# Kernel optimization log

Hardware: AMD Instinct MI355X
Metric: run time of the kernel (lower is better)

The kernel has to match this reference:

```python
import jax, jax.numpy as jnp
import numpy as np

A_ANCHORS = 102400
BATCH = 16
N_ANN = 32
OMEGA = 3.0
EPSILON = 2.0
WING_C = OMEGA - OMEGA * float(np.log(1.0 + OMEGA / EPSILON))


def _calc_iou(a, b):
    # a: [A,4] anchors, b: [N,4] gt boxes -> [A,N]
    area = (b[:, 2] - b[:, 0]) * (b[:, 3] - b[:, 1])
    iw = jnp.minimum(a[:, 2][:, None], b[None, :, 2]) - jnp.maximum(a[:, 0][:, None], b[None, :, 0])
    ih = jnp.minimum(a[:, 3][:, None], b[None, :, 3]) - jnp.maximum(a[:, 1][:, None], b[None, :, 1])
    iw = jnp.clip(iw, 0.0)
    ih = jnp.clip(ih, 0.0)
    ua = ((a[:, 2] - a[:, 0]) * (a[:, 3] - a[:, 1]))[:, None] + area[None, :] - iw * ih
    ua = jnp.clip(ua, 1e-8)
    return iw * ih / ua


def setup_inputs() -> dict:
    rng = np.random.default_rng(0)
    B, N, A = BATCH, N_ANN, A_ANCHORS
    x1 = rng.uniform(1.0, 500.0, (B, N)).astype(np.float32)
    y1 = rng.uniform(1.0, 500.0, (B, N)).astype(np.float32)
    w = rng.uniform(16.0, 100.0, (B, N)).astype(np.float32)
    h = rng.uniform(16.0, 100.0, (B, N)).astype(np.float32)
    boxes = np.stack([x1, y1, x1 + w, y1 + h], axis=-1)
    # last 12 annotations per image are padding (first coord <= 0)
    boxes[:, 20:, 0] -= 600.0
    boxes[:, 20:, 2] -= 600.0
    ldm = rng.uniform(0.0, 640.0, (B, N, 196)).astype(np.float32)
    ldm[:, ::5, :] = 0.0  # some faces have no landmark annotation
    annotations = np.concatenate([boxes, ldm], axis=-1)
    ax1 = rng.uniform(0.0, 560.0, (A,)).astype(np.float32)
    ay1 = rng.uniform(0.0, 560.0, (A,)).astype(np.float32)
    aw = rng.uniform(16.0, 80.0, (A,)).astype(np.float32)
    ah = rng.uniform(16.0, 80.0, (A,)).astype(np.float32)
    anchor = np.stack([ax1, ay1, ax1 + aw, ay1 + ah], axis=-1)
    # plant jittered copies of valid GT boxes so IoU>=0.7 positives exist
    slot = 0
    for j in range(B):
        for k in range(20):
            for _ in range(4):
                anchor[slot] = boxes[j, k] + rng.uniform(-1.5, 1.5, (4,)).astype(np.float32)
                slot += 1
    anchors = anchor[None, :, :]
    k1, k2, k3 = jax.random.split(jax.random.key(0), 3)
    return {
        "classifications": jax.random.normal(k1, (B, A, 2), jnp.float32),
        "bbox_regressions": jax.random.normal(k2, (B, A, 4), jnp.float32),
        "ldm_regressions": jax.random.normal(k3, (B, A, 196), jnp.float32),
        "anchors": jnp.asarray(anchors),
        "annotations": jnp.asarray(annotations),
    }


def reference(classifications, bbox_regressions, ldm_regressions, anchors, annotations):
    anchor = anchors[0]
    A = anchor.shape[0]
    aw = anchor[:, 2] - anchor[:, 0]
    ah = anchor[:, 3] - anchor[:, 1]
    acx = anchor[:, 0] + 0.5 * aw
    acy = anchor[:, 1] + 0.5 * ah
    bbox_scale = jnp.array([0.1, 0.1, 0.2, 0.2], jnp.float32)
    even = (jnp.arange(196) % 2) == 0
    ctr = jnp.where(even, acx[:, None], acy[:, None])         # [A,196]
    den = jnp.where(even, aw[:, None], ah[:, None]) + 1e-14   # [A,196]
    s = jnp.concatenate([jnp.ones(68, jnp.float32), 3.0 * jnp.ones(128, jnp.float32)])
    arange_A = jnp.arange(A)

    def per_sample(cls, breg, lreg, ann):
        valid = ann[:, 0] > 0
        boxes = ann[:, :4]
        ldm_ann = ann[:, 4:]
        has_gt = jnp.any(valid)
        iou = _calc_iou(anchor, boxes)
        iou = jnp.where(valid[None, :], iou, -1.0)  # mask invalid GT
        iou_max = iou.max(axis=1)
        iou_arg = iou.argmax(axis=1)
        neg = iou_max < 0.4
        pos = iou_max >= 0.7
        npos = pos.sum()
        nneg = neg.sum()
        # hard-negative mining: keep top-(3*npos) negative scores
        keep = jnp.minimum(nneg, 3 * npos)
        neg_losses = jnp.where(neg, -cls[:, 1], -jnp.inf)
        sorted_neg = jnp.sort(neg_losses)[::-1]
        neg_mean = jnp.where(arange_A < keep, sorted_neg, 0.0).sum() / jnp.maximum(keep, 1)
        pos_mean = jnp.where(pos, -cls[:, 0], 0.0).sum() / jnp.maximum(npos, 1)
        cls_loss = jnp.where(has_gt & (npos > 0), pos_mean + neg_mean, 0.0)
        gb = boxes[iou_arg]
        gw = gb[:, 2] - gb[:, 0]
        gh = gb[:, 3] - gb[:, 1]
        gcx = gb[:, 0] + 0.5 * gw
        gcy = gb[:, 1] + 0.5 * gh
        tdx = (gcx - acx) / (aw + 1e-14)
        tdy = (gcy - acy) / (ah + 1e-14)
        tdw = jnp.log(gw / aw)
        tdh = jnp.log(gh / ah)
        btgt = jnp.stack([tdx, tdy, tdw, tdh], axis=1) / bbox_scale
        d = jnp.abs(btgt - breg)
        sl1 = jnp.where(d < 1.0, 0.5 * d * d, d - 0.5)
        bbox_loss = jnp.where(
            has_gt & (npos > 0),
            jnp.where(pos[:, None], sl1, 0.0).sum() / (jnp.maximum(npos, 1) * 4),
            0.0,
        )
        # landmark wing loss over positive anchors whose GT has landmarks
        gl = ldm_ann[iou_arg]  # [A,196]
        lpos = pos & (gl.sum(axis=1) > 0)
        nl = lpos.sum()
        ltgt = (gl - ctr) / den / 0.1
        dd = jnp.abs(ltgt * s - lreg * s)
        wing = jnp.where(dd < OMEGA, OMEGA * jnp.log1p(dd / EPSILON), dd - WING_C)
        ldm_loss = jnp.where(
            has_gt & (nl > 0),
            jnp.where(lpos[:, None], wing, 0.0).sum() / (jnp.maximum(nl, 1) * 196),
            0.0,
        )
        return cls_loss, bbox_loss, ldm_loss

    return jax.vmap(per_sample)(classifications, bbox_regressions, ldm_regressions, annotations)
```

## Files before the change

kernel.cpp:

```cpp
#include <hip/hip_runtime.h>

#define A_ANCH 102400
#define BATCH  16
#define N_ANN  32
#define NLDM   196
#define ANNW   200
#define BLOCKS_PER 400
#define NSLOT  32
#define SEL_T  1024
#define CAP    14336

#define OFF_PCNT   (16u << 10)
#define OFF_PSUM   (131072u)
#define OFF_HSLOT  (294912u)
#define OFF_KEYS   (1u << 20)
#define OFF_SPILL  (8u << 20)

__device__ __forceinline__ float key_to_val(unsigned kk) {
    unsigned vb = (kk & 0x80000000u) ? (kk ^ 0x80000000u) : ~kk;
    return __uint_as_float(vb);
}

__global__ __launch_bounds__(256) void k_main(
    const float* __restrict__ cls,
    const float* __restrict__ breg,
    const float* __restrict__ lreg,
    const float* __restrict__ anchors,
    const float* __restrict__ ann,
    int4* __restrict__ pcnt,
    double* __restrict__ psum,
    unsigned* __restrict__ keys,
    unsigned* __restrict__ histS)
{
    const int tid = threadIdx.x;
    const int b = blockIdx.x / BLOCKS_PER;
    const int blk = blockIdx.x % BLOCKS_PER;
    const int a = blk * 256 + tid;

    __shared__ int    bh[256];
    __shared__ int    s_cnt[4][3];
    __shared__ double s_sum[4][3];
    bh[tid] = 0;
    __syncthreads();

    float4 av = *reinterpret_cast<const float4*>(anchors + (size_t)a * 4);
    const float aw = av.z - av.x, ah = av.w - av.y;
    const float areaA = aw * ah;

    const float* __restrict__ annb = ann + (size_t)b * N_ANN * ANNW;
    float bnum = -1e30f, bden = 1.0f; int arg = 0;
    #pragma unroll 8
    for (int j = 0; j < N_ANN; ++j) {
        float4 bx = *reinterpret_cast<const float4*>(annb + (size_t)j * ANNW);
        float areaB = (bx.z - bx.x) * (bx.w - bx.y);
        float iw = fminf(av.z, bx.z) - fmaxf(av.x, bx.x);
        float ih = fminf(av.w, bx.w) - fmaxf(av.y, bx.y);
        iw = fmaxf(iw, 0.0f); ih = fmaxf(ih, 0.0f);
        float inter = iw * ih;
        float ua = fmaxf(areaA + areaB - inter, 1e-8f);
        bool upd = inter * bden > bnum * ua;
        bnum = upd ? inter : bnum;
        bden = upd ? ua : bden;
        arg  = upd ? j : arg;
    }
    const bool pos = bnum >= 0.7f * bden;
    const bool neg = bnum <  0.4f * bden;

    float2 c = *reinterpret_cast<const float2*>(cls + ((size_t)b * A_ANCH + a) * 2);

    float nv = -c.y;
    unsigned bits = __float_as_uint(nv);
    unsigned key = (bits & 0x80000000u) ? ~bits : (bits ^ 0x80000000u);
    keys[(size_t)b * A_ANCH + a] = neg ? key : 0u;
    if (neg) atomicAdd(&bh[key >> 24], 1);

    double v_pos = 0.0, v_bb = 0.0, v_ldm = 0.0;
    float glsum = 0.0f;
    const float acx = av.x + 0.5f * aw, acy = av.y + 0.5f * ah;

    if (pos) {
        v_pos = (double)(-c.x);

        float4 gb = *reinterpret_cast<const float4*>(annb + (size_t)arg * ANNW);
        float gw = gb.z - gb.x, gh = gb.w - gb.y;
        float gcx = gb.x + 0.5f * gw, gcy = gb.y + 0.5f * gh;
        float t0 = ((gcx - acx) / (aw + 1e-14f)) / 0.1f;
        float t1 = ((gcy - acy) / (ah + 1e-14f)) / 0.1f;
        float t2 = logf(gw / aw) / 0.2f;
        float t3 = logf(gh / ah) / 0.2f;

        float4 rv = *reinterpret_cast<const float4*>(breg + ((size_t)b * A_ANCH + a) * 4);
        float bsum = 0.0f, d;
        d = fabsf(t0 - rv.x); bsum += (d < 1.0f) ? 0.5f * d * d : d - 0.5f;
        d = fabsf(t1 - rv.y); bsum += (d < 1.0f) ? 0.5f * d * d : d - 0.5f;
        d = fabsf(t2 - rv.z); bsum += (d < 1.0f) ? 0.5f * d * d : d - 0.5f;
        d = fabsf(t3 - rv.w); bsum += (d < 1.0f) ? 0.5f * d * d : d - 0.5f;
        v_bb = (double)bsum;

        const float* gl = annb + (size_t)arg * ANNW + 4;
        for (int i = 0; i < NLDM; i += 4) {
            float4 g4 = *reinterpret_cast<const float4*>(gl + i);
            glsum += g4.x + g4.y + g4.z + g4.w;
        }
    }
    const bool lpos = pos && (glsum > 0.0f);
    if (lpos) {
        const float* gl = annb + (size_t)arg * ANNW + 4;
        const float* lr = lreg + ((size_t)b * A_ANCH + a) * NLDM;
        const float inv_aw = 1.0f / ((aw + 1e-14f) * 0.1f);
        const float inv_ah = 1.0f / ((ah + 1e-14f) * 0.1f);
        double wsum = 0.0;
        for (int i = 0; i < NLDM; i += 4) {
            float4 l4 = *reinterpret_cast<const float4*>(lr + i);
            float4 g4 = *reinterpret_cast<const float4*>(gl + i);
            float s = (i < 68) ? 1.0f : 3.0f;
            float lt0 = (g4.x - acx) * inv_aw;
            float lt1 = (g4.y - acy) * inv_ah;
            float lt2 = (g4.z - acx) * inv_aw;
            float lt3 = (g4.w - acy) * inv_ah;
            float d0 = fabsf(lt0 * s - l4.x * s);
            float d1 = fabsf(lt1 * s - l4.y * s);
            float d2 = fabsf(lt2 * s - l4.z * s);
            float d3 = fabsf(lt3 * s - l4.w * s);
            float w0 = (d0 < 3.0f) ? 3.0f * log1pf(d0 * 0.5f) : d0 - 0.25112780437753474f;
            float w1 = (d1 < 3.0f) ? 3.0f * log1pf(d1 * 0.5f) : d1 - 0.25112780437753474f;
            float w2 = (d2 < 3.0f) ? 3.0f * log1pf(d2 * 0.5f) : d2 - 0.25112780437753474f;
            float w3 = (d3 < 3.0f) ? 3.0f * log1pf(d3 * 0.5f) : d3 - 0.25112780437753474f;
            wsum += (double)w0 + (double)w1 + (double)w2 + (double)w3;
        }
        v_ldm = wsum;
    }

    unsigned long long bp = __ballot(pos);
    unsigned long long bn = __ballot(neg);
    unsigned long long bl = __ballot(lpos);
    const int wave = tid >> 6, lane = tid & 63;
    if (lane == 0) {
        s_cnt[wave][0] = (int)__popcll(bp);
        s_cnt[wave][1] = (int)__popcll(bn);
        s_cnt[wave][2] = (int)__popcll(bl);
    }
    if (bp) {
        #pragma unroll
        for (int off = 32; off > 0; off >>= 1) {
            v_pos += __shfl_down(v_pos, off);
            v_bb  += __shfl_down(v_bb, off);
            v_ldm += __shfl_down(v_ldm, off);
        }
    }
    if (lane == 0) {
        s_sum[wave][0] = v_pos;
        s_sum[wave][1] = v_bb;
        s_sum[wave][2] = v_ldm;
    }
    __syncthreads();
    if (tid == 0) {
        int np = s_cnt[0][0] + s_cnt[1][0] + s_cnt[2][0] + s_cnt[3][0];
        int nn = s_cnt[0][1] + s_cnt[1][1] + s_cnt[2][1] + s_cnt[3][1];
        int nl = s_cnt[0][2] + s_cnt[1][2] + s_cnt[2][2] + s_cnt[3][2];
        pcnt[b * BLOCKS_PER + blk] = make_int4(np, nn, nl, 0);
        size_t pbase = (size_t)(b * BLOCKS_PER + blk) * 3;
        psum[pbase + 0] = s_sum[0][0] + s_sum[1][0] + s_sum[2][0] + s_sum[3][0];
        psum[pbase + 1] = s_sum[0][1] + s_sum[1][1] + s_sum[2][1] + s_sum[3][1];
        psum[pbase + 2] = s_sum[0][2] + s_sum[1][2] + s_sum[2][2] + s_sum[3][2];
    }
    if (bh[tid]) {
        unsigned slot = (unsigned)(blockIdx.x & (NSLOT - 1));
        atomicAdd(&histS[((unsigned)b * NSLOT + slot) * 256u + (unsigned)tid],
                  (unsigned)bh[tid]);
    }
}

__global__ __launch_bounds__(SEL_T) void k_sel(
    const float* __restrict__ ann,
    const int4* __restrict__ pcnt,
    const double* __restrict__ psum,
    const unsigned* __restrict__ histS,
    const unsigned* __restrict__ keys,
    unsigned* __restrict__ spill,
    float* __restrict__ out)
{
    const int b = blockIdx.x;
    const int tid = threadIdx.x;
    const int wave = tid >> 6, lane = tid & 63;

    __shared__ unsigned shist[256];
    __shared__ unsigned s_cand[CAP];
    __shared__ int    sredi[16][3];
    __shared__ double sredd[16][3];
    __shared__ int    s_i[8];
    __shared__ double s_d[4];
    __shared__ unsigned s_prefix;
    __shared__ int s_r;
    __shared__ int s_cc;

    if (tid < 256) {
        unsigned h = 0;
        #pragma unroll
        for (int s = 0; s < NSLOT; ++s)
            h += histS[((unsigned)b * NSLOT + s) * 256u + (unsigned)tid];
        shist[tid] = h;
    }

    int np = 0, nn = 0, nl = 0;
    double a0 = 0.0, a1 = 0.0, a2 = 0.0;
    for (int i = tid; i < BLOCKS_PER; i += SEL_T) {
        int4 p = pcnt[b * BLOCKS_PER + i];
        np += p.x; nn += p.y; nl += p.z;
        size_t pbase = (size_t)(b * BLOCKS_PER + i) * 3;
        a0 += psum[pbase + 0]; a1 += psum[pbase + 1]; a2 += psum[pbase + 2];
    }
    #pragma unroll
    for (int off = 32; off > 0; off >>= 1) {
        np += __shfl_down(np, off); nn += __shfl_down(nn, off); nl += __shfl_down(nl, off);
        a0 += __shfl_down(a0, off); a1 += __shfl_down(a1, off); a2 += __shfl_down(a2, off);
    }
    if (lane == 0) {
        sredi[wave][0] = np; sredi[wave][1] = nn; sredi[wave][2] = nl;
        sredd[wave][0] = a0; sredd[wave][1] = a1; sredd[wave][2] = a2;
    }

    if (tid < 64) {
        bool v = (tid < N_ANN) && (ann[(size_t)(b * N_ANN + tid) * ANNW] > 0.0f);
        unsigned long long bm = __ballot(v);
        if (tid == 0) s_i[6] = (bm != 0ull) ? 1 : 0;
    }
    __syncthreads();

    if (tid == 0) {
        int tnp = 0, tnn = 0, tnl = 0; double t0 = 0, t1 = 0, t2 = 0;
        for (int w = 0; w < 16; ++w) {
            tnp += sredi[w][0]; tnn += sredi[w][1]; tnl += sredi[w][2];
            t0 += sredd[w][0]; t1 += sredd[w][1]; t2 += sredd[w][2];
        }
        int keep = min(tnn, 3 * tnp);
        int bin0 = -1, rem = 0;
        if (keep > 0) {
            unsigned cum = 0;
            for (int i = 255; i >= 0; --i) {
                unsigned cc = shist[i];
                if (cum + cc >= (unsigned)keep) { bin0 = i; rem = keep - (int)cum; break; }
                cum += cc;
            }
        }
        s_i[0] = tnp; s_i[1] = tnn; s_i[2] = tnl;
        s_i[3] = keep; s_i[4] = bin0; s_i[5] = rem;
        s_d[0] = t0; s_d[1] = t1; s_d[2] = t2;
        s_cc = 0;
    }
    __syncthreads();

    const int keep = s_i[3];
    const int bin0 = s_i[4];
    unsigned* sp = spill + (size_t)b * A_ANCH;

    double lneg = 0.0;
    if (keep > 0) {
        const uint4* k4 = reinterpret_cast<const uint4*>(keys + (size_t)b * A_ANCH);
        const unsigned long long lmask = (1ull << lane) - 1ull;
        for (int i = tid; i < A_ANCH / 4; i += SEL_T) {
            uint4 kv = k4[i];
            #pragma unroll
            for (int e = 0; e < 4; ++e) {
                unsigned kk = (e == 0) ? kv.x : (e == 1) ? kv.y : (e == 2) ? kv.z : kv.w;
                int top = (int)(kk >> 24);
                if (top > bin0) lneg += (double)key_to_val(kk);
                bool m = (top == bin0);
                unsigned long long bm = __ballot(m);
                if (bm) {
                    int ldr = __ffsll((long long)bm) - 1;
                    int base = 0;
                    if (lane == ldr) base = atomicAdd(&s_cc, (int)__popcll(bm));
                    base = __shfl(base, ldr);
                    if (m) {
                        int idx = base + (int)__popcll(bm & lmask);
                        if (idx < CAP) s_cand[idx] = kk;
                        else sp[idx - CAP] = kk;
                    }
                }
            }
        }
    }
    #pragma unroll
    for (int off = 32; off > 0; off >>= 1) lneg += __shfl_down(lneg, off);
    __syncthreads();
    if (lane == 0) sredd[wave][0] = lneg;
    __syncthreads();
    if (tid == 0) {
        double t = 0.0;
        for (int w = 0; w < 16; ++w) t += sredd[w][0];
        s_d[3] = t;
        s_i[7] = s_cc;
    }
    __syncthreads();
    const int cnt = s_i[7];

    unsigned prefix = ((unsigned)bin0) << 24;
    for (int pass = 1; pass < 4; ++pass) {
        const int shift = 24 - 8 * pass;
        const unsigned maskAbove = 0xFFFFFFFFu << (shift + 8);
        if (tid < 256) shist[tid] = 0;
        __syncthreads();
        for (int i = tid; i < cnt; i += SEL_T) {
            unsigned kk = (i < CAP) ? s_cand[i] : sp[i - CAP];
            if ((kk & maskAbove) == prefix)
                atomicAdd(&shist[(kk >> shift) & 0xFFu], 1u);
        }
        __syncthreads();
        if (tid == 0) {
            int rem = (pass == 1) ? s_i[5] : s_r;
            unsigned cum = 0;
            unsigned npre = prefix;
            int nrem = rem;
            for (int bin = 255; bin >= 0; --bin) {
                unsigned cc = shist[bin];
                if (cum + cc >= (unsigned)rem) {
                    nrem = rem - (int)cum;
                    npre = prefix | ((unsigned)bin << shift);
                    break;
                }
                cum += cc;
            }
            s_r = nrem; s_prefix = npre;
        }
        __syncthreads();
        prefix = s_prefix;
    }
    const unsigned T = prefix;

    double ls = 0.0;
    for (int i = tid; i < cnt; i += SEL_T) {
        unsigned kk = (i < CAP) ? s_cand[i] : sp[i - CAP];
        if (kk > T) ls += (double)key_to_val(kk);
    }
    #pragma unroll
    for (int off = 32; off > 0; off >>= 1) ls += __shfl_down(ls, off);
    __syncthreads();
    if (lane == 0) sredd[wave][0] = ls;
    __syncthreads();

    if (tid == 0) {
        double cs = 0.0;
        for (int w = 0; w < 16; ++w) cs += sredd[w][0];
        double total = s_d[3] + cs + (double)s_r * (double)key_to_val(T);

        const int npos = s_i[0], nlc = s_i[2], hasgt = s_i[6];
        double cls_l = 0.0, bbox_l = 0.0, ldm_l = 0.0;
        if (hasgt && npos > 0) {
            double neg_mean = (keep > 0) ? total / (double)keep : 0.0;
            cls_l = s_d[0] / (double)npos + neg_mean;
            bbox_l = s_d[1] / ((double)npos * 4.0);
        }
        if (hasgt && nlc > 0) {
            ldm_l = s_d[2] / ((double)nlc * 196.0);
        }
        out[b]             = (float)cls_l;
        out[BATCH + b]     = (float)bbox_l;
        out[2 * BATCH + b] = (float)ldm_l;
    }
}

extern "C" void kernel_launch(void* const* d_in, const int* in_sizes, int n_in,
                              void* d_out, int out_size, void* d_ws, size_t ws_size,
                              hipStream_t stream) {
    const float* cls     = (const float*)d_in[0];
    const float* breg    = (const float*)d_in[1];
    const float* lreg    = (const float*)d_in[2];
    const float* anchors = (const float*)d_in[3];
    const float* ann     = (const float*)d_in[4];

    char* ws = (char*)d_ws;
    int4*     pcnt  = (int4*)(ws + OFF_PCNT);
    double*   psum  = (double*)(ws + OFF_PSUM);
    unsigned* histS = (unsigned*)(ws + OFF_HSLOT);
    unsigned* keys  = (unsigned*)(ws + OFF_KEYS);
    unsigned* spill = (unsigned*)(ws + OFF_SPILL);
    float*    out   = (float*)d_out;

    hipMemsetAsync(histS, 0, (size_t)BATCH * NSLOT * 256 * 4, stream);
    hipLaunchKernelGGL(k_main, dim3(BATCH * BLOCKS_PER), dim3(256), 0, stream,
                       cls, breg, lreg, anchors, ann, pcnt, psum, keys, histS);
    hipLaunchKernelGGL(k_sel, dim3(BATCH), dim3(SEL_T), 0, stream,
                       ann, pcnt, psum, histS, keys, spill, out);
}
```

Before: 157.6 us.

## Fuse anchor-matching and hard-negative selection into one kernel via last-block-done

Merges the per-anchor loss kernel and the per-image top-k selection kernel into a single launch. Each block now loops over 1600 anchors (64 blocks per image) and writes its own histogram slice instead of doing global atomics. The last block to finish an image, detected with an atomic counter, performs the radix selection. The selection now runs with 256 threads instead of 1024 and keeps candidates in global memory rather than shared memory, which may slow the serial tail. The grid is also much smaller (1024 blocks), which could reduce parallelism in the memory-bound main phase.

Measured after the change: 333.2 us. 2.11x slower.

```diff
diff --git a/kernel.cpp b/kernel.cpp
--- a/kernel.cpp
+++ b/kernel.cpp
@@ -5,260 +5,236 @@
 #define N_ANN  32
 #define NLDM   196
 #define ANNW   200
-#define BLOCKS_PER 400
-#define NSLOT  32
-#define SEL_T  1024
-#define CAP    14336
-
-#define OFF_PCNT   (16u << 10)
-#define OFF_PSUM   (131072u)
-#define OFF_HSLOT  (294912u)
-#define OFF_KEYS   (1u << 20)
-#define OFF_SPILL  (8u << 20)
+#define NB     64
+#define APB    1600
+#define WING_CONST 0.25112780437753474f
+
+#define OFF_DONE   0u
+#define OFF_PCNT   4096u
+#define OFF_PSUM   (64u << 10)
+#define OFF_BHIST  (128u << 10)
+#define OFF_KEYS   (2u << 20)
+#define OFF_CAND   (16u << 20)
 
 __device__ __forceinline__ float key_to_val(unsigned kk) {
     unsigned vb = (kk & 0x80000000u) ? (kk ^ 0x80000000u) : ~kk;
     return __uint_as_float(vb);
 }
 
-__global__ __launch_bounds__(256) void k_main(
+__global__ __launch_bounds__(256, 4) void k_fused(
     const float* __restrict__ cls,
     const float* __restrict__ breg,
     const float* __restrict__ lreg,
     const float* __restrict__ anchors,
     const float* __restrict__ ann,
+    int* __restrict__ done,
     int4* __restrict__ pcnt,
     double* __restrict__ psum,
+    unsigned* __restrict__ bhist,
     unsigned* __restrict__ keys,
-    unsigned* __restrict__ histS)
+    unsigned* __restrict__ cand,
+    float* __restrict__ out)
 {
     const int tid = threadIdx.x;
-    const int b = blockIdx.x / BLOCKS_PER;
-    const int blk = blockIdx.x % BLOCKS_PER;
-    const int a = blk * 256 + tid;
+    const int b   = blockIdx.x / NB;
+    const int blk = blockIdx.x % NB;
+    const int base = blk * APB;
+    const int wave = tid >> 6, lane = tid & 63;
 
     __shared__ int    bh[256];
-    __shared__ int    s_cnt[4][3];
-    __shared__ double s_sum[4][3];
+    __shared__ int    sci[4][3];
+    __shared__ double scd[4][3];
+    __shared__ int    s_flag;
     bh[tid] = 0;
     __syncthreads();
 
-    float4 av = *reinterpret_cast<const float4*>(anchors + (size_t)a * 4);
-    const float aw = av.z - av.x, ah = av.w - av.y;
-    const float areaA = aw * ah;
-
     const float* __restrict__ annb = ann + (size_t)b * N_ANN * ANNW;
-    float bnum = -1e30f, bden = 1.0f; int arg = 0;
-    #pragma unroll 8
-    for (int j = 0; j < N_ANN; ++j) {
-        float4 bx = *reinterpret_cast<const float4*>(annb + (size_t)j * ANNW);
-        float areaB = (bx.z - bx.x) * (bx.w - bx.y);
-        float iw = fminf(av.z, bx.z) - fmaxf(av.x, bx.x);
-        float ih = fminf(av.w, bx.w) - fmaxf(av.y, bx.y);
-        iw = fmaxf(iw, 0.0f); ih = fmaxf(ih, 0.0f);
-        float inter = iw * ih;
-        float ua = fmaxf(areaA + areaB - inter, 1e-8f);
-        bool upd = inter * bden > bnum * ua;
-        bnum = upd ? inter : bnum;
-        bden = upd ? ua : bden;
-        arg  = upd ? j : arg;
-    }
-    const bool pos = bnum >= 0.7f * bden;
-    const bool neg = bnum <  0.4f * bden;
-
-    float2 c = *reinterpret_cast<const float2*>(cls + ((size_t)b * A_ANCH + a) * 2);
-
-    float nv = -c.y;
-    unsigned bits = __float_as_uint(nv);
-    unsigned key = (bits & 0x80000000u) ? ~bits : (bits ^ 0x80000000u);
-    keys[(size_t)b * A_ANCH + a] = neg ? key : 0u;
-    if (neg) atomicAdd(&bh[key >> 24], 1);
-
-    double v_pos = 0.0, v_bb = 0.0, v_ldm = 0.0;
-    float glsum = 0.0f;
-    const float acx = av.x + 0.5f * aw, acy = av.y + 0.5f * ah;
-
-    if (pos) {
-        v_pos = (double)(-c.x);
-
-        float4 gb = *reinterpret_cast<const float4*>(annb + (size_t)arg * ANNW);
-        float gw = gb.z - gb.x, gh = gb.w - gb.y;
-        float gcx = gb.x + 0.5f * gw, gcy = gb.y + 0.5f * gh;
-        float t0 = ((gcx - acx) / (aw + 1e-14f)) / 0.1f;
-        float t1 = ((gcy - acy) / (ah + 1e-14f)) / 0.1f;
-        float t2 = logf(gw / aw) / 0.2f;
-        float t3 = logf(gh / ah) / 0.2f;
-
-        float4 rv = *reinterpret_cast<const float4*>(breg + ((size_t)b * A_ANCH + a) * 4);
-        float bsum = 0.0f, d;
-        d = fabsf(t0 - rv.x); bsum += (d < 1.0f) ? 0.5f * d * d : d - 0.5f;
-        d = fabsf(t1 - rv.y); bsum += (d < 1.0f) ? 0.5f * d * d : d - 0.5f;
-        d = fabsf(t2 - rv.z); bsum += (d < 1.0f) ? 0.5f * d * d : d - 0.5f;
-        d = fabsf(t3 - rv.w); bsum += (d < 1.0f) ? 0.5f * d * d : d - 0.5f;
-        v_bb = (double)bsum;
-
-        const float* gl = annb + (size_t)arg * ANNW + 4;
-        for (int i = 0; i < NLDM; i += 4) {
-            float4 g4 = *reinterpret_cast<const float4*>(gl + i);
-            glsum += g4.x + g4.y + g4.z + g4.w;
-        }
-    }
-    const bool lpos = pos && (glsum > 0.0f);
-    if (lpos) {
-        const float* gl = annb + (size_t)arg * ANNW + 4;
-        const float* lr = lreg + ((size_t)b * A_ANCH + a) * NLDM;
-        const float inv_aw = 1.0f / ((aw + 1e-14f) * 0.1f);
-        const float inv_ah = 1.0f / ((ah + 1e-14f) * 0.1f);
-        double wsum = 0.0;
-        for (int i = 0; i < NLDM; i += 4) {
-            float4 l4 = *reinterpret_cast<const float4*>(lr + i);
-            float4 g4 = *reinterpret_cast<const float4*>(gl + i);
-            float s = (i < 68) ? 1.0f : 3.0f;
-            float lt0 = (g4.x - acx) * inv_aw;
-            float lt1 = (g4.y - acy) * inv_ah;
-            float lt2 = (g4.z - acx) * inv_aw;
-            float lt3 = (g4.w - acy) * inv_ah;
-            float d0 = fabsf(lt0 * s - l4.x * s);
-            float d1 = fabsf(lt1 * s - l4.y * s);
-            float d2 = fabsf(lt2 * s - l4.z * s);
-            float d3 = fabsf(lt3 * s - l4.w * s);
-            float w0 = (d0 < 3.0f) ? 3.0f * log1pf(d0 * 0.5f) : d0 - 0.25112780437753474f;
-            float w1 = (d1 < 3.0f) ? 3.0f * log1pf(d1 * 0.5f) : d1 - 0.25112780437753474f;
-            float w2 = (d2 < 3.0f) ? 3.0f * log1pf(d2 * 0.5f) : d2 - 0.25112780437753474f;
-            float w3 = (d3 < 3.0f) ? 3.0f * log1pf(d3 * 0.5f) : d3 - 0.25112780437753474f;
-            wsum += (double)w0 + (double)w1 + (double)w2 + (double)w3;
-        }
-        v_ldm = wsum;
-    }
-
-    unsigned long long bp = __ballot(pos);
-    unsigned long long bn = __ballot(neg);
-    unsigned long long bl = __ballot(lpos);
-    const int wave = tid >> 6, lane = tid & 63;
+
+    int np = 0, nn = 0, nl = 0;
+    double vp = 0.0, vb = 0.0, vl = 0.0;
+
+    #pragma unroll 1
+    for (int off = tid; off < APB; off += 256) {
+        const int a = base + off;
+        float4 av = *reinterpret_cast<const float4*>(anchors + (size_t)a * 4);
+        const float aw = av.z - av.x, ah = av.w - av.y;
+        const float areaA = aw * ah;
+
+        float bnum = -1e30f, bden = 1.0f; int arg = 0;
+        #pragma unroll 8
+        for (int j = 0; j < N_ANN; ++j) {
+            float4 bx = *reinterpret_cast<const float4*>(annb + (size_t)j * ANNW);
+            float areaB = (bx.z - bx.x) * (bx.w - bx.y);
+            float iw = fminf(av.z, bx.z) - fmaxf(av.x, bx.x);
+            float ih = fminf(av.w, bx.w) - fmaxf(av.y, bx.y);
+            iw = fmaxf(iw, 0.0f); ih = fmaxf(ih, 0.0f);
+            float inter = iw * ih;
+            float ua = fmaxf(areaA + areaB - inter, 1e-8f);
+            bool upd = inter * bden > bnum * ua;
+            bnum = upd ? inter : bnum;
+            bden = upd ? ua : bden;
+            arg  = upd ? j : arg;
+        }
+        const bool pos = bnum >= 0.7f * bden;
+        const bool neg = bnum <  0.4f * bden;
+
+        float2 c = *reinterpret_cast<const float2*>(cls + ((size_t)b * A_ANCH + a) * 2);
+
+        float nv = -c.y;
+        unsigned bits = __float_as_uint(nv);
+        unsigned key = (bits & 0x80000000u) ? ~bits : (bits ^ 0x80000000u);
+        keys[(size_t)b * A_ANCH + a] = neg ? key : 0u;
+        if (neg) { atomicAdd(&bh[key >> 24], 1); nn++; }
+
+        if (pos) {
+            np++;
+            vp += (double)(-c.x);
+
+            const float acx = av.x + 0.5f * aw, acy = av.y + 0.5f * ah;
+            float4 gb = *reinterpret_cast<const float4*>(annb + (size_t)arg * ANNW);
+            float gw = gb.z - gb.x, gh = gb.w - gb.y;
+            float gcx = gb.x + 0.5f * gw, gcy = gb.y + 0.5f * gh;
+            float t0 = ((gcx - acx) / (aw + 1e-14f)) / 0.1f;
+            float t1 = ((gcy - acy) / (ah + 1e-14f)) / 0.1f;
+            float t2 = logf(gw / aw) / 0.2f;
+            float t3 = logf(gh / ah) / 0.2f;
+
+            float4 rv = *reinterpret_cast<const float4*>(breg + ((size_t)b * A_ANCH + a) * 4);
+            float bsum = 0.0f, d;
+            d = fabsf(t0 - rv.x); bsum += (d < 1.0f) ? 0.5f * d * d : d - 0.5f;
+            d = fabsf(t1 - rv.y); bsum += (d < 1.0f) ? 0.5f * d * d : d - 0.5f;
+            d = fabsf(t2 - rv.z); bsum += (d < 1.0f) ? 0.5f * d * d : d - 0.5f;
+            d = fabsf(t3 - rv.w); bsum += (d < 1.0f) ? 0.5f * d * d : d - 0.5f;
+            vb += (double)bsum;
+
+            const float* gl = annb + (size_t)arg * ANNW + 4;
+            float glsum = 0.0f;
+            for (int i = 0; i < NLDM; i += 4) {
+                float4 g4 = *reinterpret_cast<const float4*>(gl + i);
+                glsum += g4.x + g4.y + g4.z + g4.w;
+            }
+            if (glsum > 0.0f) {
+                nl++;
+                const float* lr = lreg + ((size_t)b * A_ANCH + a) * NLDM;
+                const float inv_aw = 1.0f / ((aw + 1e-14f) * 0.1f);
+                const float inv_ah = 1.0f / ((ah + 1e-14f) * 0.1f);
+                double wsum = 0.0;
+                for (int i = 0; i < NLDM; i += 4) {
+                    float4 l4 = *reinterpret_cast<const float4*>(lr + i);
+                    float4 g4 = *reinterpret_cast<const float4*>(gl + i);
+                    float s = (i < 68) ? 1.0f : 3.0f;
+                    float lt0 = (g4.x - acx) * inv_aw;
+                    float lt1 = (g4.y - acy) * inv_ah;
+                    float lt2 = (g4.z - acx) * inv_aw;
+                    float lt3 = (g4.w - acy) * inv_ah;
+                    float d0 = fabsf(lt0 * s - l4.x * s);
+                    float d1 = fabsf(lt1 * s - l4.y * s);
+                    float d2 = fabsf(lt2 * s - l4.z * s);
+                    float d3 = fabsf(lt3 * s - l4.w * s);
+                    float w0 = (d0 < 3.0f) ? 3.0f * log1pf(d0 * 0.5f) : d0 - WING_CONST;
+                    float w1 = (d1 < 3.0f) ? 3.0f * log1pf(d1 * 0.5f) : d1 - WING_CONST;
+                    float w2 = (d2 < 3.0f) ? 3.0f * log1pf(d2 * 0.5f) : d2 - WING_CONST;
+                    float w3 = (d3 < 3.0f) ? 3.0f * log1pf(d3 * 0.5f) : d3 - WING_CONST;
+                    wsum += (double)w0 + (double)w1 + (double)w2 + (double)w3;
+                }
+                vl += wsum;
+            }
+        }
+    }
+
+    #pragma unroll
+    for (int o = 32; o > 0; o >>= 1) {
+        np += __shfl_down(np, o); nn += __shfl_down(nn, o); nl += __shfl_down(nl, o);
+        vp += __shfl_down(vp, o); vb += __shfl_down(vb, o); vl += __shfl_down(vl, o);
+    }
     if (lane == 0) {
-        s_cnt[wave][0] = (int)__popcll(bp);
-        s_cnt[wave][1] = (int)__popcll(bn);
-        s_cnt[wave][2] = (int)__popcll(bl);
-    }
-    if (bp) {
-        #pragma unroll
-        for (int off = 32; off > 0; off >>= 1) {
-            v_pos += __shfl_down(v_pos, off);
-            v_bb  += __shfl_down(v_bb, off);
-            v_ldm += __shfl_down(v_ldm, off);
-        }
-    }
-    if (lane == 0) {
-        s_sum[wave][0] = v_pos;
-        s_sum[wave][1] = v_bb;
-        s_sum[wave][2] = v_ldm;
+        sci[wave][0] = np; sci[wave][1] = nn; sci[wave][2] = nl;
+        scd[wave][0] = vp; scd[wave][1] = vb; scd[wave][2] = vl;
     }
     __syncthreads();
     if (tid == 0) {
-        int np = s_cnt[0][0] + s_cnt[1][0] + s_cnt[2][0] + s_cnt[3][0];
-        int nn = s_cnt[0][1] + s_cnt[1][1] + s_cnt[2][1] + s_cnt[3][1];
-        int nl = s_cnt[0][2] + s_cnt[1][2] + s_cnt[2][2] + s_cnt[3][2];
-        pcnt[b * BLOCKS_PER + blk] = make_int4(np, nn, nl, 0);
-        size_t pbase = (size_t)(b * BLOCKS_PER + blk) * 3;
-        psum[pbase + 0] = s_sum[0][0] + s_sum[1][0] + s_sum[2][0] + s_sum[3][0];
-        psum[pbase + 1] = s_sum[0][1] + s_sum[1][1] + s_sum[2][1] + s_sum[3][1];
-        psum[pbase + 2] = s_sum[0][2] + s_sum[1][2] + s_sum[2][2] + s_sum[3][2];
-    }
-    if (bh[tid]) {
-        unsigned slot = (unsigned)(blockIdx.x & (NSLOT - 1));
-        atomicAdd(&histS[((unsigned)b * NSLOT + slot) * 256u + (unsigned)tid],
-                  (unsigned)bh[tid]);
-    }
-}
-
-__global__ __launch_bounds__(SEL_T) void k_sel(
-    const float* __restrict__ ann,
-    const int4* __restrict__ pcnt,
-    const double* __restrict__ psum,
-    const unsigned* __restrict__ histS,
-    const unsigned* __restrict__ keys,
-    unsigned* __restrict__ spill,
-    float* __restrict__ out)
-{
-    const int b = blockIdx.x;
-    const int tid = threadIdx.x;
-    const int wave = tid >> 6, lane = tid & 63;
+        int tnp = sci[0][0] + sci[1][0] + sci[2][0] + sci[3][0];
+        int tnn = sci[0][1] + sci[1][1] + sci[2][1] + sci[3][1];
+        int tnl = sci[0][2] + sci[1][2] + sci[2][2] + sci[3][2];
+        pcnt[b * NB + blk] = make_int4(tnp, tnn, tnl, 0);
+        size_t pb = (size_t)(b * NB + blk) * 3;
+        psum[pb + 0] = scd[0][0] + scd[1][0] + scd[2][0] + scd[3][0];
+        psum[pb + 1] = scd[0][1] + scd[1][1] + scd[2][1] + scd[3][1];
+        psum[pb + 2] = scd[0][2] + scd[1][2] + scd[2][2] + scd[3][2];
+    }
+    bhist[(unsigned)((b * NB + blk) << 8) + (unsigned)tid] = (unsigned)bh[tid];
+
+    __threadfence();
+    __syncthreads();
+    if (tid == 0) {
+        int old = atomicAdd(&done[b], 1);
+        s_flag = (old == NB - 1) ? 1 : 0;
+    }
+    __syncthreads();
+    if (!s_flag) return;
+    __threadfence();
 
     __shared__ unsigned shist[256];
-    __shared__ unsigned s_cand[CAP];
-    __shared__ int    sredi[16][3];
-    __shared__ double sredd[16][3];
     __shared__ int    s_i[8];
-    __shared__ double s_d[4];
+    __shared__ double s_d[5];
     __shared__ unsigned s_prefix;
     __shared__ int s_r;
     __shared__ int s_cc;
-
-    if (tid < 256) {
-        unsigned h = 0;
+    __shared__ double sredd[4];
+
+    unsigned h = 0;
+    #pragma unroll 8
+    for (int k = 0; k < NB; ++k)
+        h += bhist[(unsigned)((b * NB + k) << 8) + (unsigned)tid];
+    shist[tid] = h;
+
+    if (tid >= 64 && tid < 128) {
+        int j = tid - 64;
+        bool v = (j < N_ANN) && (annb[(size_t)j * ANNW] > 0.0f);
+        unsigned long long bm = __ballot(v);
+        if (tid == 64) s_i[6] = (bm != 0ull) ? 1 : 0;
+    }
+    __syncthreads();
+
+    if (tid < 64) {
+        int4 p = pcnt[b * NB + tid];
+        size_t pb = (size_t)(b * NB + tid) * 3;
+        int xnp = p.x, xnn = p.y, xnl = p.z;
+        double a0 = psum[pb], a1 = psum[pb + 1], a2 = psum[pb + 2];
         #pragma unroll
-        for (int s = 0; s < NSLOT; ++s)
-            h += histS[((unsigned)b * NSLOT + s) * 256u + (unsigned)tid];
-        shist[tid] = h;
-    }
-
-    int np = 0, nn = 0, nl = 0;
-    double a0 = 0.0, a1 = 0.0, a2 = 0.0;
-    for (int i = tid; i < BLOCKS_PER; i += SEL_T) {
-        int4 p = pcnt[b * BLOCKS_PER + i];
-        np += p.x; nn += p.y; nl += p.z;
-        size_t pbase = (size_t)(b * BLOCKS_PER + i) * 3;
-        a0 += psum[pbase + 0]; a1 += psum[pbase + 1]; a2 += psum[pbase + 2];
-    }
-    #pragma unroll
-    for (int off = 32; off > 0; off >>= 1) {
-        np += __shfl_down(np, off); nn += __shfl_down(nn, off); nl += __shfl_down(nl, off);
-        a0 += __shfl_down(a0, off); a1 += __shfl_down(a1, off); a2 += __shfl_down(a2, off);
-    }
-    if (lane == 0) {
-        sredi[wave][0] = np; sredi[wave][1] = nn; sredi[wave][2] = nl;
-        sredd[wave][0] = a0; sredd[wave][1] = a1; sredd[wave][2] = a2;
-    }
-
-    if (tid < 64) {
-        bool v = (tid < N_ANN) && (ann[(size_t)(b * N_ANN + tid) * ANNW] > 0.0f);
-        unsigned long long bm = __ballot(v);
-        if (tid == 0) s_i[6] = (bm != 0ull) ? 1 : 0;
-    }
-    __syncthreads();
-
-    if (tid == 0) {
-        int tnp = 0, tnn = 0, tnl = 0; double t0 = 0, t1 = 0, t2 = 0;
-        for (int w = 0; w < 16; ++w) {
-            tnp += sredi[w][0]; tnn += sredi[w][1]; tnl += sredi[w][2];
-            t0 += sredd[w][0]; t1 += sredd[w][1]; t2 += sredd[w][2];
-        }
-        int keep = min(tnn, 3 * tnp);
-        int bin0 = -1, rem = 0;
-        if (keep > 0) {
-            unsigned cum = 0;
-            for (int i = 255; i >= 0; --i) {
-                unsigned cc = shist[i];
-                if (cum + cc >= (unsigned)keep) { bin0 = i; rem = keep - (int)cum; break; }
-                cum += cc;
-            }
-        }
-        s_i[0] = tnp; s_i[1] = tnn; s_i[2] = tnl;
-        s_i[3] = keep; s_i[4] = bin0; s_i[5] = rem;
-        s_d[0] = t0; s_d[1] = t1; s_d[2] = t2;
-        s_cc = 0;
+        for (int o = 32; o > 0; o >>= 1) {
+            xnp += __shfl_down(xnp, o); xnn += __shfl_down(xnn, o); xnl += __shfl_down(xnl, o);
+            a0 += __shfl_down(a0, o); a1 += __shfl_down(a1, o); a2 += __shfl_down(a2, o);
+        }
+        if (tid == 0) {
+            int keep = min(xnn, 3 * xnp);
+            int bin0 = -1, rem = 0;
+            if (keep > 0) {
+                unsigned cum = 0;
+                for (int i = 255; i >= 0; --i) {
+                    unsigned cc = shist[i];
+                    if (cum + cc >= (unsigned)keep) { bin0 = i; rem = keep - (int)cum; break; }
+                    cum += cc;
+                }
+            }
+            s_i[0] = xnp; s_i[1] = xnn; s_i[2] = xnl;
+            s_i[3] = keep; s_i[4] = bin0; s_i[5] = rem;
+            s_d[0] = a0; s_d[1] = a1; s_d[2] = a2;
+            s_d[4] = 0.0;
+            s_cc = 0;
+        }
     }
     __syncthreads();
 
     const int keep = s_i[3];
     const int bin0 = s_i[4];
-    unsigned* sp = spill + (size_t)b * A_ANCH;
-
-    double lneg = 0.0;
-    if (keep > 0) {
+    unsigned* cd = cand + (size_t)b * A_ANCH;
+
+    if (keep > 0 && bin0 >= 0) {
+        double lneg = 0.0;
         const uint4* k4 = reinterpret_cast<const uint4*>(keys + (size_t)b * A_ANCH);
         const unsigned long long lmask = (1ull << lane) - 1ull;
-        for (int i = tid; i < A_ANCH / 4; i += SEL_T) {
+        for (int i = tid; i < A_ANCH / 4; i += 256) {
             uint4 kv = k4[i];
             #pragma unroll
             for (int e = 0; e < 4; ++e) {
@@ -269,82 +245,74 @@
                 unsigned long long bm = __ballot(m);
                 if (bm) {
                     int ldr = __ffsll((long long)bm) - 1;
-                    int base = 0;
-                    if (lane == ldr) base = atomicAdd(&s_cc, (int)__popcll(bm));
-                    base = __shfl(base, ldr);
-                    if (m) {
-                        int idx = base + (int)__popcll(bm & lmask);
-                        if (idx < CAP) s_cand[idx] = kk;
-                        else sp[idx - CAP] = kk;
+                    int bs = 0;
+                    if (lane == ldr) bs = atomicAdd(&s_cc, (int)__popcll(bm));
+                    bs = __shfl(bs, ldr);
+                    if (m) cd[bs + (int)__popcll(bm & lmask)] = kk;
+                }
+            }
+        }
+        #pragma unroll
+        for (int o = 32; o > 0; o >>= 1) lneg += __shfl_down(lneg, o);
+        if (lane == 0) sredd[wave] = lneg;
+        __syncthreads();
+        if (tid == 0) {
+            s_d[3] = sredd[0] + sredd[1] + sredd[2] + sredd[3];
+            s_i[7] = s_cc;
+        }
+        __syncthreads();
+        const int cnt = s_i[7];
+
+        unsigned prefix = ((unsigned)bin0) << 24;
+        for (int pass = 1; pass < 4; ++pass) {
+            const int shift = 24 - 8 * pass;
+            const unsigned maskAbove = 0xFFFFFFFFu << (shift + 8);
+            shist[tid] = 0;
+            __syncthreads();
+            for (int i = tid; i < cnt; i += 256) {
+                unsigned kk = cd[i];
+                if ((kk & maskAbove) == prefix)
+                    atomicAdd(&shist[(kk >> shift) & 0xFFu], 1u);
+            }
+            __syncthreads();
+            if (tid == 0) {
+                int rem = (pass == 1) ? s_i[5] : s_r;
+                unsigned cum = 0; unsigned npre = prefix; int nrem = rem;
+                for (int bin = 255; bin >= 0; --bin) {
+                    unsigned cc = shist[bin];
+                    if (cum + cc >= (unsigned)rem) {
+                        nrem = rem - (int)cum;
+                        npre = prefix | ((unsigned)bin << shift);
+                        break;
                     }
+                    cum += cc;
                 }
-            }
-        }
-    }
-    #pragma unroll
-    for (int off = 32; off > 0; off >>= 1) lneg += __shfl_down(lneg, off);
-    __syncthreads();
-    if (lane == 0) sredd[wave][0] = lneg;
-    __syncthreads();
+                s_r = nrem; s_prefix = npre;
+            }
+            __syncthreads();
+            prefix = s_prefix;
+        }
+        const unsigned T = prefix;
+
+        double ls = 0.0;
+        for (int i = tid; i < cnt; i += 256) {
+            unsigned kk = cd[i];
+            if (kk > T) ls += (double)key_to_val(kk);
+        }
+        #pragma unroll
+        for (int o = 32; o > 0; o >>= 1) ls += __shfl_down(ls, o);
+        __syncthreads();
+        if (lane == 0) sredd[wave] = ls;
+        __syncthreads();
+        if (tid == 0)
+            s_d[4] = s_d[3] + sredd[0] + sredd[1] + sredd[2] + sredd[3]
+                   + (double)s_r * (double)key_to_val(T);
+        __syncthreads();
+    }
+
     if (tid == 0) {
-        double t = 0.0;
-        for (int w = 0; w < 16; ++w) t += sredd[w][0];
-        s_d[3] = t;
-        s_i[7] = s_cc;
-    }
-    __syncthreads();
-    const int cnt = s_i[7];
-
-    unsigned prefix = ((unsigned)bin0) << 24;
-    for (int pass = 1; pass < 4; ++pass) {
-        const int shift = 24 - 8 * pass;
-        const unsigned maskAbove = 0xFFFFFFFFu << (shift + 8);
-        if (tid < 256) shist[tid] = 0;
-        __syncthreads();
-        for (int i = tid; i < cnt; i += SEL_T) {
-            unsigned kk = (i < CAP) ? s_cand[i] : sp[i - CAP];
-            if ((kk & maskAbove) == prefix)
-                atomicAdd(&shist[(kk >> shift) & 0xFFu], 1u);
-        }
-        __syncthreads();
-        if (tid == 0) {
-            int rem = (pass == 1) ? s_i[5] : s_r;
-            unsigned cum = 0;
-            unsigned npre = prefix;
-            int nrem = rem;
-            for (int bin = 255; bin >= 0; --bin) {
-                unsigned cc = shist[bin];
-                if (cum + cc >= (unsigned)rem) {
-                    nrem = rem - (int)cum;
-                    npre = prefix | ((unsigned)bin << shift);
-                    break;
-                }
-                cum += cc;
-            }
-            s_r = nrem; s_prefix = npre;
-        }
-        __syncthreads();
-        prefix = s_prefix;
-    }
-    const unsigned T = prefix;
-
-    double ls = 0.0;
-    for (int i = tid; i < cnt; i += SEL_T) {
-        unsigned kk = (i < CAP) ? s_cand[i] : sp[i - CAP];
-        if (kk > T) ls += (double)key_to_val(kk);
-    }
-    #pragma unroll
-    for (int off = 32; off > 0; off >>= 1) ls += __shfl_down(ls, off);
-    __syncthreads();
-    if (lane == 0) sredd[wave][0] = ls;
-    __syncthreads();
-
-    if (tid == 0) {
-        double cs = 0.0;
-        for (int w = 0; w < 16; ++w) cs += sredd[w][0];
-        double total = s_d[3] + cs + (double)s_r * (double)key_to_val(T);
-
         const int npos = s_i[0], nlc = s_i[2], hasgt = s_i[6];
+        const double total = s_d[4];
         double cls_l = 0.0, bbox_l = 0.0, ldm_l = 0.0;
         if (hasgt && npos > 0) {
             double neg_mean = (keep > 0) ? total / (double)keep : 0.0;
@@ -370,16 +338,16 @@
     const float* ann     = (const float*)d_in[4];
 
     char* ws = (char*)d_ws;
+    int*      done  = (int*)(ws + OFF_DONE);
     int4*     pcnt  = (int4*)(ws + OFF_PCNT);
     double*   psum  = (double*)(ws + OFF_PSUM);
-    unsigned* histS = (unsigned*)(ws + OFF_HSLOT);
+    unsigned* bhist = (unsigned*)(ws + OFF_BHIST);
     unsigned* keys  = (unsigned*)(ws + OFF_KEYS);
-    unsigned* spill = (unsigned*)(ws + OFF_SPILL);
+    unsigned* cand  = (unsigned*)(ws + OFF_CAND);
     float*    out   = (float*)d_out;
 
-    hipMemsetAsync(histS, 0, (size_t)BATCH * NSLOT * 256 * 4, stream);
-    hipLaunchKernelGGL(k_main, dim3(BATCH * BLOCKS_PER), dim3(256), 0, stream,
-                       cls, breg, lreg, anchors, ann, pcnt, psum, keys, histS);
-    hipLaunchKernelGGL(k_sel, dim3(BATCH), dim3(SEL_T), 0, stream,
-                       ann, pcnt, psum, histS, keys, spill, out);
+    hipMemsetAsync(done, 0, BATCH * sizeof(int), stream);
+    hipLaunchKernelGGL(k_fused, dim3(BATCH * NB), dim3(256), 0, stream,
+                       cls, breg, lreg, anchors, ann,
+                       done, pcnt, psum, bhist, keys, cand, out);
 }
```
